# Kernel optimization log

Measured on AMD Instinct MI355X. Metric: run time of the kernel, lower is better.

## Reference

```python
import jax, jax.numpy as jnp
import numpy as np

N_SPK, N_UTT, D_EMB = 1024, 20, 512
COS_EPS = 1e-8   # torch F.cosine_similarity default eps
SIM_EPS = 1e-6   # added to cosine and inside the log, per original code


def setup_inputs() -> dict:
    key = jax.random.key(0)
    embeddings = jax.random.normal(key, (N_SPK, N_UTT, D_EMB), dtype=jnp.float32)
    w = jnp.asarray(10.0, dtype=jnp.float32)
    b = jnp.asarray(-5.0, dtype=jnp.float32)
    return {"embeddings": embeddings, "w": w, "b": b}


def reference(embeddings, w, b):
    N, M, D = embeddings.shape
    sums = embeddings.sum(axis=1)                       # [N, D]
    centroids = sums / M                                # [N, D] full centroids
    cent_excl = (sums[:, None, :] - embeddings) / (M - 1)  # [N, M, D] leave-one-out

    def _norm(x):
        return x / jnp.maximum(jnp.linalg.norm(x, axis=-1, keepdims=True), COS_EPS)

    e_n = _norm(embeddings)          # [N, M, D]
    c_n = _norm(centroids)           # [N, D]
    ce_n = _norm(cent_excl)          # [N, M, D]

    # cosine vs every speaker centroid
    cs = jnp.einsum('nmd,kd->nmk', e_n, c_n)            # [N, M, N]
    # replace same-speaker column with leave-one-out cosine
    diag = jnp.sum(e_n * ce_n, axis=-1)                 # [N, M]
    same = jnp.eye(N, dtype=bool)[:, None, :]           # [N, 1, N]
    cossim = jnp.where(same, diag[:, :, None], cs) + SIM_EPS

    sim = w * cossim + b                                # [N, M, N]
    pos = w * (diag + SIM_EPS) + b                      # sim[j, i, j]
    lse = jnp.log(jnp.sum(jnp.exp(sim), axis=-1) + SIM_EPS)  # [N, M]
    loss = jnp.sum(lse - pos)
    return loss
```

## Files before the change

kernel.cpp:

```cpp
#include <hip/hip_runtime.h>
#include <hip/hip_bf16.h>

typedef unsigned short u16;
typedef unsigned int u32;
typedef unsigned char u8;
typedef int i32x8 __attribute__((ext_vector_type(8)));
typedef float f32x4 __attribute__((ext_vector_type(4)));

#define NSPK 1024
#define NUTT 20
#define DEMB 512
#define NROW (NSPK * NUTT)

__device__ __forceinline__ uint2 pk_fp8x8(float a, float b, float c, float d,
                                          float e, float f, float g, float h) {
    int lo = __builtin_amdgcn_cvt_pk_fp8_f32(a, b, 0, 0);
    lo = __builtin_amdgcn_cvt_pk_fp8_f32(c, d, lo, 1);
    int hi = __builtin_amdgcn_cvt_pk_fp8_f32(e, f, 0, 0);
    hi = __builtin_amdgcn_cvt_pk_fp8_f32(g, h, hi, 1);
    return make_uint2((u32)lo, (u32)hi);
}

__global__ __launch_bounds__(256) void prep_f(const float* __restrict__ E,
                                              u8* __restrict__ A,
                                              u8* __restrict__ Bc,
                                              float* __restrict__ diag,
                                              float* __restrict__ csd,
                                              float* __restrict__ rs,
                                              float* __restrict__ out) {
    __shared__ float sbuf[4][DEMB];
    const int t = threadIdx.x, lane = t & 63, wv = t >> 6;
    const int n = blockIdx.x;
    const float* Eb = E + (size_t)n * (NUTT * DEMB) + (size_t)(wv * 5) * DEMB + lane * 8;

    float4 e0[5], e1[5];
    float4 p0 = {0, 0, 0, 0}, p1 = {0, 0, 0, 0};
#pragma unroll
    for (int i = 0; i < 5; ++i) {
        e0[i] = *(const float4*)(Eb + (size_t)i * DEMB);
        e1[i] = *(const float4*)(Eb + (size_t)i * DEMB + 4);
        p0.x += e0[i].x; p0.y += e0[i].y; p0.z += e0[i].z; p0.w += e0[i].w;
        p1.x += e1[i].x; p1.y += e1[i].y; p1.z += e1[i].z; p1.w += e1[i].w;
    }
    *(float4*)(&sbuf[wv][lane * 8])     = p0;
    *(float4*)(&sbuf[wv][lane * 8 + 4]) = p1;
    __syncthreads();

    float4 s0 = {0, 0, 0, 0}, s1 = {0, 0, 0, 0};
#pragma unroll
    for (int k = 0; k < 4; ++k) {
        float4 a = *(const float4*)(&sbuf[k][lane * 8]);
        float4 b = *(const float4*)(&sbuf[k][lane * 8 + 4]);
        s0.x += a.x; s0.y += a.y; s0.z += a.z; s0.w += a.w;
        s1.x += b.x; s1.y += b.y; s1.z += b.z; s1.w += b.w;
    }

    float ls = s0.x*s0.x + s0.y*s0.y + s0.z*s0.z + s0.w*s0.w
             + s1.x*s1.x + s1.y*s1.y + s1.z*s1.z + s1.w*s1.w;
#pragma unroll
    for (int o = 32; o; o >>= 1) ls += __shfl_xor(ls, o);
    const float ss = ls;
    const float rc = 1.0f / fmaxf(sqrtf(ss) * 0.05f, 1e-8f);
    const float g  = rc * 0.05f;

    ((uint2*)(Bc + (size_t)n * DEMB))[lane] =
        pk_fp8x8(s0.x * g, s0.y * g, s0.z * g, s0.w * g,
                 s1.x * g, s1.y * g, s1.z * g, s1.w * g);

#pragma unroll
    for (int i = 0; i < 5; ++i) {
        float ee = e0[i].x*e0[i].x + e0[i].y*e0[i].y + e0[i].z*e0[i].z + e0[i].w*e0[i].w
                 + e1[i].x*e1[i].x + e1[i].y*e1[i].y + e1[i].z*e1[i].z + e1[i].w*e1[i].w;
        float es = e0[i].x*s0.x + e0[i].y*s0.y + e0[i].z*s0.z + e0[i].w*s0.w
                 + e1[i].x*s1.x + e1[i].y*s1.y + e1[i].z*s1.z + e1[i].w*s1.w;
#pragma unroll
        for (int o = 32; o; o >>= 1) { ee += __shfl_xor(ee, o); es += __shfl_xor(es, o); }

        const float rne = 1.0f / fmaxf(sqrtf(ee), 1e-8f);
        const float pxx = ss - 2.f * es + ee;
        const float dg  = (es - ee) * rne / fmaxf(sqrtf(pxx), 1.9e-7f);

        const int r = n * NUTT + wv * 5 + i;
        ((uint2*)(A + (size_t)r * DEMB))[lane] =
            pk_fp8x8(e0[i].x * rne, e0[i].y * rne, e0[i].z * rne, e0[i].w * rne,
                     e1[i].x * rne, e1[i].y * rne, e1[i].z * rne, e1[i].w * rne);
        if (lane == 0) {
            diag[r] = dg;
            csd[r]  = es * g * rne;
        }
    }

    if (t < NUTT) rs[n * NUTT + t] = 0.f;
    if (n == 0 && t == 0) out[0] = 0.f;
}

__device__ __forceinline__ void async_copy16(const void* g, void* l) {
    __builtin_amdgcn_global_load_lds(
        (const __attribute__((address_space(1))) void*)g,
        (__attribute__((address_space(3))) void*)l, 16, 0, 0);
}

__global__ __launch_bounds__(256) void gemm_mx(const u8* __restrict__ A,
                                               const u8* __restrict__ Bc,
                                               const float* __restrict__ wp,
                                               const float* __restrict__ bp,
                                               float* __restrict__ rowsum) {
    __shared__ u8 As[128 * 128];
    __shared__ u8 Bs[128 * 128];
    const int t = threadIdx.x;
    const int lane = t & 63, wv = t >> 6;
    const int ml = lane & 15, q = lane >> 4;
    const int wm = wv >> 1, wn = wv & 1;
    const int tileM = blockIdx.x;
    const int tileN = blockIdx.y;

    const float w = *wp, bb = *bp;

    const u8* Ag = A + (size_t)tileM * 128 * DEMB;
    const u8* Bg = Bc + (size_t)tileN * 128 * DEMB;

    const u8* asrc[4]; const u8* bsrc[4]; u8* adst[4]; u8* bdst[4];
#pragma unroll
    for (int j = 0; j < 4; ++j) {
        const int c = t + 256 * j;
        const int r = c >> 3, kg = (c & 7) ^ (r & 7);
        asrc[j] = Ag + (size_t)r * DEMB + kg * 16;  adst[j] = As + c * 16;
        bsrc[j] = Bg + (size_t)r * DEMB + kg * 16;  bdst[j] = Bs + c * 16;
    }

    int a0[4], a1[4], b0[4], b1[4];
#pragma unroll
    for (int i = 0; i < 4; ++i) {
        const int r = wm * 64 + i * 16 + ml;
        const int c = wn * 64 + i * 16 + ml;
        a0[i] = r * 128 + (((2 * q)     ^ (r & 7)) << 4);
        a1[i] = r * 128 + (((2 * q + 1) ^ (r & 7)) << 4);
        b0[i] = c * 128 + (((2 * q)     ^ (c & 7)) << 4);
        b1[i] = c * 128 + (((2 * q + 1) ^ (c & 7)) << 4);
    }

    f32x4 acc[4][4];
#pragma unroll
    for (int i = 0; i < 4; ++i)
#pragma unroll
        for (int j = 0; j < 4; ++j) acc[i][j] = (f32x4){0.f, 0.f, 0.f, 0.f};

    for (int kt = 0; kt < DEMB; kt += 128) {
        __syncthreads();
#pragma unroll
        for (int j = 0; j < 4; ++j) async_copy16(asrc[j] + kt, adst[j]);
#pragma unroll
        for (int j = 0; j < 4; ++j) async_copy16(bsrc[j] + kt, bdst[j]);
        __syncthreads();

        i32x8 af[4], bf[4];
#pragma unroll
        for (int i = 0; i < 4; ++i) {
            uint4 x = *(const uint4*)(As + a0[i]);
            uint4 y = *(const uint4*)(As + a1[i]);
            af[i] = (i32x8){(int)x.x, (int)x.y, (int)x.z, (int)x.w,
                            (int)y.x, (int)y.y, (int)y.z, (int)y.w};
        }
#pragma unroll
        for (int j = 0; j < 4; ++j) {
            uint4 x = *(const uint4*)(Bs + b0[j]);
            uint4 y = *(const uint4*)(Bs + b1[j]);
            bf[j] = (i32x8){(int)x.x, (int)x.y, (int)x.z, (int)x.w,
                            (int)y.x, (int)y.y, (int)y.z, (int)y.w};
        }
#pragma unroll
        for (int i = 0; i < 4; ++i)
#pragma unroll
            for (int j = 0; j < 4; ++j)
                acc[i][j] = __builtin_amdgcn_mfma_scale_f32_16x16x128_f8f6f4(
                    af[i], bf[j], acc[i][j], 0, 0,
                    0, 0x7F7F7F7F, 0, 0x7F7F7F7F);
    }

#pragma unroll
    for (int i = 0; i < 4; ++i) {
        float s0 = 0.f, s1 = 0.f, s2 = 0.f, s3 = 0.f;
#pragma unroll
        for (int j = 0; j < 4; ++j) {
            s0 += __expf(fmaf(w, acc[i][j][0] + 1e-6f, bb));
            s1 += __expf(fmaf(w, acc[i][j][1] + 1e-6f, bb));
            s2 += __expf(fmaf(w, acc[i][j][2] + 1e-6f, bb));
            s3 += __expf(fmaf(w, acc[i][j][3] + 1e-6f, bb));
        }
#pragma unroll
        for (int o = 1; o < 16; o <<= 1) {
            s0 += __shfl_xor(s0, o); s1 += __shfl_xor(s1, o);
            s2 += __shfl_xor(s2, o); s3 += __shfl_xor(s3, o);
        }
        if (ml < 4) {
            float sv = (ml == 0) ? s0 : (ml == 1) ? s1 : (ml == 2) ? s2 : s3;
            int grow = tileM * 128 + wm * 64 + i * 16 + q * 4 + ml;
            atomicAdd(&rowsum[grow], sv);
        }
    }
}

__global__ __launch_bounds__(256) void finalize(const float* __restrict__ rowsum,
                                                const float* __restrict__ diag,
                                                const float* __restrict__ csd,
                                                const float* __restrict__ wp,
                                                const float* __restrict__ bp,
                                                float* __restrict__ out) {
    __shared__ float s_red[4];
    const int r = blockIdx.x * 256 + threadIdx.x;
    const float w = *wp, bb = *bp;
    const float dg = diag[r];
    const float pos = fmaf(w, dg + 1e-6f, bb);
    const float S = rowsum[r] - __expf(fmaf(w, csd[r] + 1e-6f, bb)) + __expf(pos);
    float term = __logf(S + 1e-6f) - pos;
    const int lane = threadIdx.x & 63, wv = threadIdx.x >> 6;
#pragma unroll
    for (int o = 32; o; o >>= 1) term += __shfl_xor(term, o);
    if (lane == 0) s_red[wv] = term;
    __syncthreads();
    if (threadIdx.x == 0) atomicAdd(out, s_red[0] + s_red[1] + s_red[2] + s_red[3]);
}

extern "C" void kernel_launch(void* const* d_in, const int* in_sizes, int n_in,
                              void* d_out, int out_size, void* d_ws, size_t ws_size,
                              hipStream_t stream) {
    const float* E = (const float*)d_in[0];
    const float* wp = (const float*)d_in[1];
    const float* bp = (const float*)d_in[2];
    float* out = (float*)d_out;

    char* ws = (char*)d_ws;
    u8* A      = (u8*)(ws);
    u8* Bc     = (u8*)(ws + 10485760);
    float* dg  = (float*)(ws + 11010048);
    float* cs  = (float*)(ws + 11091968);
    float* rs  = (float*)(ws + 11173888);

    prep_f<<<NSPK, 256, 0, stream>>>(E, A, Bc, dg, cs, rs, out);
    gemm_mx<<<dim3(160, 8), 256, 0, stream>>>(A, Bc, wp, bp, rs);
    finalize<<<80, 256, 0, stream>>>(rs, dg, cs, wp, bp, out);
}
```

Measured before the change: 109.1 us.

## Double-buffer GEMM LDS tiles and replace rowsum atomics with partial-sum buffer

The fp8 MFMA GEMM kernel now uses two LDS buffers per operand and issues the next K-tile's async global-to-LDS copies before computing on the current one. Explicit vmcnt waits and barriers replace the two per-iteration syncthreads, so memory loads overlap MFMA work. Row sums are no longer accumulated with atomicAdd. Each (tileN, wn) pair writes its partial sum to a 16-way buffer that finalize reduces, and this also removes the zeroing in prep. LDS use doubles to 64KB per block, which may lower occupancy, and the finalize kernel now does 16 extra reads per row.

```diff
diff --git a/kernel.cpp b/kernel.cpp
--- a/kernel.cpp
+++ b/kernel.cpp
@@ -26,7 +26,6 @@
                                               u8* __restrict__ Bc,
                                               float* __restrict__ diag,
                                               float* __restrict__ csd,
-                                              float* __restrict__ rs,
                                               float* __restrict__ out) {
     __shared__ float sbuf[4][DEMB];
     const int t = threadIdx.x, lane = t & 63, wv = t >> 6;
@@ -90,7 +89,6 @@
         }
     }
 
-    if (t < NUTT) rs[n * NUTT + t] = 0.f;
     if (n == 0 && t == 0) out[0] = 0.f;
 }
 
@@ -104,9 +102,9 @@
                                                const u8* __restrict__ Bc,
                                                const float* __restrict__ wp,
                                                const float* __restrict__ bp,
-                                               float* __restrict__ rowsum) {
-    __shared__ u8 As[128 * 128];
-    __shared__ u8 Bs[128 * 128];
+                                               float* __restrict__ rs16) {
+    __shared__ u8 As[2][128 * 128];
+    __shared__ u8 Bs[2][128 * 128];
     const int t = threadIdx.x;
     const int lane = t & 63, wv = t >> 6;
     const int ml = lane & 15, q = lane >> 4;
@@ -114,18 +112,27 @@
     const int tileM = blockIdx.x;
     const int tileN = blockIdx.y;
 
-    const float w = *wp, bb = *bp;
-
     const u8* Ag = A + (size_t)tileM * 128 * DEMB;
     const u8* Bg = Bc + (size_t)tileN * 128 * DEMB;
 
-    const u8* asrc[4]; const u8* bsrc[4]; u8* adst[4]; u8* bdst[4];
+    const u8* asrc[4]; const u8* bsrc[4]; int coff[4];
 #pragma unroll
     for (int j = 0; j < 4; ++j) {
         const int c = t + 256 * j;
         const int r = c >> 3, kg = (c & 7) ^ (r & 7);
-        asrc[j] = Ag + (size_t)r * DEMB + kg * 16;  adst[j] = As + c * 16;
-        bsrc[j] = Bg + (size_t)r * DEMB + kg * 16;  bdst[j] = Bs + c * 16;
+        asrc[j] = Ag + (size_t)r * DEMB + kg * 16;
+        bsrc[j] = Bg + (size_t)r * DEMB + kg * 16;
+        coff[j] = c * 16;
+    }
+
+#define STAGE(KT, BUF)                                                        \
+    {                                                                         \
+        _Pragma("unroll")                                                     \
+        for (int j = 0; j < 4; ++j)                                           \
+            async_copy16(asrc[j] + (KT) * 128, &As[BUF][coff[j]]);            \
+        _Pragma("unroll")                                                     \
+        for (int j = 0; j < 4; ++j)                                           \
+            async_copy16(bsrc[j] + (KT) * 128, &Bs[BUF][coff[j]]);            \
     }
 
     int a0[4], a1[4], b0[4], b1[4];
@@ -145,26 +152,19 @@
 #pragma unroll
         for (int j = 0; j < 4; ++j) acc[i][j] = (f32x4){0.f, 0.f, 0.f, 0.f};
 
-    for (int kt = 0; kt < DEMB; kt += 128) {
-        __syncthreads();
-#pragma unroll
-        for (int j = 0; j < 4; ++j) async_copy16(asrc[j] + kt, adst[j]);
-#pragma unroll
-        for (int j = 0; j < 4; ++j) async_copy16(bsrc[j] + kt, bdst[j]);
-        __syncthreads();
-
+    auto compute = [&](int buf) {
         i32x8 af[4], bf[4];
 #pragma unroll
         for (int i = 0; i < 4; ++i) {
-            uint4 x = *(const uint4*)(As + a0[i]);
-            uint4 y = *(const uint4*)(As + a1[i]);
+            uint4 x = *(const uint4*)(&As[buf][a0[i]]);
+            uint4 y = *(const uint4*)(&As[buf][a1[i]]);
             af[i] = (i32x8){(int)x.x, (int)x.y, (int)x.z, (int)x.w,
                             (int)y.x, (int)y.y, (int)y.z, (int)y.w};
         }
 #pragma unroll
         for (int j = 0; j < 4; ++j) {
-            uint4 x = *(const uint4*)(Bs + b0[j]);
-            uint4 y = *(const uint4*)(Bs + b1[j]);
+            uint4 x = *(const uint4*)(&Bs[buf][b0[j]]);
+            uint4 y = *(const uint4*)(&Bs[buf][b1[j]]);
             bf[j] = (i32x8){(int)x.x, (int)x.y, (int)x.z, (int)x.w,
                             (int)y.x, (int)y.y, (int)y.z, (int)y.w};
         }
@@ -175,8 +175,44 @@
                 acc[i][j] = __builtin_amdgcn_mfma_scale_f32_16x16x128_f8f6f4(
                     af[i], bf[j], acc[i][j], 0, 0,
                     0, 0x7F7F7F7F, 0, 0x7F7F7F7F);
-    }
-
+    };
+
+#define PHASE_END()                                            \
+    asm volatile("s_waitcnt lgkmcnt(0)" ::: "memory");         \
+    __builtin_amdgcn_sched_barrier(0);                         \
+    __builtin_amdgcn_s_barrier();                              \
+    __builtin_amdgcn_sched_barrier(0);
+
+#define WAIT_TILE(N)                                           \
+    asm volatile("s_waitcnt vmcnt(" #N ")" ::: "memory");      \
+    __builtin_amdgcn_sched_barrier(0);                         \
+    __builtin_amdgcn_s_barrier();                              \
+    __builtin_amdgcn_sched_barrier(0);
+
+    STAGE(0, 0);
+    STAGE(1, 1);
+    WAIT_TILE(8);
+    compute(0);
+    PHASE_END();
+
+    STAGE(2, 0);
+    WAIT_TILE(8);
+    compute(1);
+    PHASE_END();
+
+    STAGE(3, 1);
+    WAIT_TILE(8);
+    compute(0);
+    PHASE_END();
+
+    WAIT_TILE(0);
+    compute(1);
+
+#undef STAGE
+#undef PHASE_END
+#undef WAIT_TILE
+
+    const float w = *wp, bb = *bp;
 #pragma unroll
     for (int i = 0; i < 4; ++i) {
         float s0 = 0.f, s1 = 0.f, s2 = 0.f, s3 = 0.f;
@@ -195,12 +231,12 @@
         if (ml < 4) {
             float sv = (ml == 0) ? s0 : (ml == 1) ? s1 : (ml == 2) ? s2 : s3;
             int grow = tileM * 128 + wm * 64 + i * 16 + q * 4 + ml;
-            atomicAdd(&rowsum[grow], sv);
-        }
-    }
-}
-
-__global__ __launch_bounds__(256) void finalize(const float* __restrict__ rowsum,
+            rs16[((size_t)tileN * 2 + wn) * NROW + grow] = sv;
+        }
+    }
+}
+
+__global__ __launch_bounds__(256) void finalize(const float* __restrict__ rs16,
                                                 const float* __restrict__ diag,
                                                 const float* __restrict__ csd,
                                                 const float* __restrict__ wp,
@@ -209,9 +245,12 @@
     __shared__ float s_red[4];
     const int r = blockIdx.x * 256 + threadIdx.x;
     const float w = *wp, bb = *bp;
+    float rsum = 0.f;
+#pragma unroll
+    for (int p = 0; p < 16; ++p) rsum += rs16[(size_t)p * NROW + r];
     const float dg = diag[r];
     const float pos = fmaf(w, dg + 1e-6f, bb);
-    const float S = rowsum[r] - __expf(fmaf(w, csd[r] + 1e-6f, bb)) + __expf(pos);
+    const float S = rsum - __expf(fmaf(w, csd[r] + 1e-6f, bb)) + __expf(pos);
     float term = __logf(S + 1e-6f) - pos;
     const int lane = threadIdx.x & 63, wv = threadIdx.x >> 6;
 #pragma unroll
@@ -234,9 +273,9 @@
     u8* Bc     = (u8*)(ws + 10485760);
     float* dg  = (float*)(ws + 11010048);
     float* cs  = (float*)(ws + 11091968);
-    float* rs  = (float*)(ws + 11173888);
-
-    prep_f<<<NSPK, 256, 0, stream>>>(E, A, Bc, dg, cs, rs, out);
-    gemm_mx<<<dim3(160, 8), 256, 0, stream>>>(A, Bc, wp, bp, rs);
-    finalize<<<80, 256, 0, stream>>>(rs, dg, cs, wp, bp, out);
-}
+    float* rs16 = (float*)(ws + 11173888);
+
+    prep_f<<<NSPK, 256, 0, stream>>>(E, A, Bc, dg, cs, out);
+    gemm_mx<<<dim3(160, 8), 256, 0, stream>>>(A, Bc, wp, bp, rs16);
+    finalize<<<80, 256, 0, stream>>>(rs16, dg, cs, wp, bp, out);
+}
```

Result: no change. 107.1 us (-1.8%).

## Fuse GEMM and finalize with register-resident A rows and double-buffered B streaming

Applied to the files above, without the earlier changes.

Replaces the 2D-tiled GEMM plus separate finalize kernel with one kernel of 256 blocks. Each block keeps 80 full fp8 embedding rows resident in registers and streams all 1024 centroids through a double-buffered LDS pipeline with explicit waitcnt and barrier control. Row sums of exp stay in registers, which removes the rowsum atomics, the zeroing in prep and the finalize launch. The trade-off is one block per CU with heavy register use, and only 256 blocks to spread across the CUs.

```diff
diff --git a/kernel.cpp b/kernel.cpp
--- a/kernel.cpp
+++ b/kernel.cpp
@@ -26,7 +26,6 @@
                                               u8* __restrict__ Bc,
                                               float* __restrict__ diag,
                                               float* __restrict__ csd,
-                                              float* __restrict__ rs,
                                               float* __restrict__ out) {
     __shared__ float sbuf[4][DEMB];
     const int t = threadIdx.x, lane = t & 63, wv = t >> 6;
@@ -90,7 +89,6 @@
         }
     }
 
-    if (t < NUTT) rs[n * NUTT + t] = 0.f;
     if (n == 0 && t == 0) out[0] = 0.f;
 }
 
@@ -100,125 +98,181 @@
         (__attribute__((address_space(3))) void*)l, 16, 0, 0);
 }
 
-__global__ __launch_bounds__(256) void gemm_mx(const u8* __restrict__ A,
-                                               const u8* __restrict__ Bc,
-                                               const float* __restrict__ wp,
-                                               const float* __restrict__ bp,
-                                               float* __restrict__ rowsum) {
-    __shared__ u8 As[128 * 128];
-    __shared__ u8 Bs[128 * 128];
-    const int t = threadIdx.x;
-    const int lane = t & 63, wv = t >> 6;
+__global__ __launch_bounds__(256, 1) void gemm_fin(const u8* __restrict__ A,
+                                                   const u8* __restrict__ Bc,
+                                                   const float* __restrict__ wp,
+                                                   const float* __restrict__ bp,
+                                                   const float* __restrict__ diag,
+                                                   const float* __restrict__ csd,
+                                                   float* __restrict__ out) {
+    __shared__ u8 As[80 * DEMB];
+    __shared__ u8 Bs[2][128 * 128];
+    __shared__ float red[4][80];
+    __shared__ float s_red[4];
+    const int t = threadIdx.x, lane = t & 63, wv = t >> 6;
     const int ml = lane & 15, q = lane >> 4;
-    const int wm = wv >> 1, wn = wv & 1;
-    const int tileM = blockIdx.x;
-    const int tileN = blockIdx.y;
+    const int blk = blockIdx.x;
+    const u8* Ag = A + (size_t)blk * 80 * DEMB;
 
     const float w = *wp, bb = *bp;
-
-    const u8* Ag = A + (size_t)tileM * 128 * DEMB;
-    const u8* Bg = Bc + (size_t)tileN * 128 * DEMB;
-
-    const u8* asrc[4]; const u8* bsrc[4]; u8* adst[4]; u8* bdst[4];
+    asm volatile("s_waitcnt vmcnt(0) lgkmcnt(0)" ::: "memory");
+
+    int boff[4];
 #pragma unroll
     for (int j = 0; j < 4; ++j) {
         const int c = t + 256 * j;
         const int r = c >> 3, kg = (c & 7) ^ (r & 7);
-        asrc[j] = Ag + (size_t)r * DEMB + kg * 16;  adst[j] = As + c * 16;
-        bsrc[j] = Bg + (size_t)r * DEMB + kg * 16;  bdst[j] = Bs + c * 16;
-    }
-
-    int a0[4], a1[4], b0[4], b1[4];
-#pragma unroll
-    for (int i = 0; i < 4; ++i) {
-        const int r = wm * 64 + i * 16 + ml;
-        const int c = wn * 64 + i * 16 + ml;
-        a0[i] = r * 128 + (((2 * q)     ^ (r & 7)) << 4);
-        a1[i] = r * 128 + (((2 * q + 1) ^ (r & 7)) << 4);
-        b0[i] = c * 128 + (((2 * q)     ^ (c & 7)) << 4);
-        b1[i] = c * 128 + (((2 * q + 1) ^ (c & 7)) << 4);
-    }
-
-    f32x4 acc[4][4];
-#pragma unroll
-    for (int i = 0; i < 4; ++i)
-#pragma unroll
-        for (int j = 0; j < 4; ++j) acc[i][j] = (f32x4){0.f, 0.f, 0.f, 0.f};
-
-    for (int kt = 0; kt < DEMB; kt += 128) {
-        __syncthreads();
-#pragma unroll
-        for (int j = 0; j < 4; ++j) async_copy16(asrc[j] + kt, adst[j]);
-#pragma unroll
-        for (int j = 0; j < 4; ++j) async_copy16(bsrc[j] + kt, bdst[j]);
-        __syncthreads();
-
-        i32x8 af[4], bf[4];
-#pragma unroll
-        for (int i = 0; i < 4; ++i) {
-            uint4 x = *(const uint4*)(As + a0[i]);
-            uint4 y = *(const uint4*)(As + a1[i]);
-            af[i] = (i32x8){(int)x.x, (int)x.y, (int)x.z, (int)x.w,
-                            (int)y.x, (int)y.y, (int)y.z, (int)y.w};
-        }
-#pragma unroll
-        for (int j = 0; j < 4; ++j) {
-            uint4 x = *(const uint4*)(Bs + b0[j]);
-            uint4 y = *(const uint4*)(Bs + b1[j]);
-            bf[j] = (i32x8){(int)x.x, (int)x.y, (int)x.z, (int)x.w,
-                            (int)y.x, (int)y.y, (int)y.z, (int)y.w};
-        }
-#pragma unroll
-        for (int i = 0; i < 4; ++i)
-#pragma unroll
-            for (int j = 0; j < 4; ++j)
-                acc[i][j] = __builtin_amdgcn_mfma_scale_f32_16x16x128_f8f6f4(
-                    af[i], bf[j], acc[i][j], 0, 0,
-                    0, 0x7F7F7F7F, 0, 0x7F7F7F7F);
-    }
-
-#pragma unroll
-    for (int i = 0; i < 4; ++i) {
-        float s0 = 0.f, s1 = 0.f, s2 = 0.f, s3 = 0.f;
-#pragma unroll
-        for (int j = 0; j < 4; ++j) {
-            s0 += __expf(fmaf(w, acc[i][j][0] + 1e-6f, bb));
-            s1 += __expf(fmaf(w, acc[i][j][1] + 1e-6f, bb));
-            s2 += __expf(fmaf(w, acc[i][j][2] + 1e-6f, bb));
-            s3 += __expf(fmaf(w, acc[i][j][3] + 1e-6f, bb));
-        }
+        boff[j] = r * DEMB + kg * 16;
+    }
+
+    auto stageB = [&](int tileN, int kt, u8* buf) {
+#pragma unroll
+        for (int j = 0; j < 4; ++j)
+            async_copy16(Bc + (size_t)tileN * (128 * DEMB) + kt * 128 + boff[j],
+                         buf + t * 16 + j * 4096);
+    };
+
+#pragma unroll
+    for (int jj = 0; jj < 10; ++jj) {
+        const int c = t + 256 * jj;
+        const int r = c >> 5, sl = c & 31;
+        async_copy16(Ag + (size_t)r * DEMB + ((sl ^ (r & 31)) << 4),
+                     As + t * 16 + jj * 4096);
+    }
+    stageB(0, 0, Bs[0]);
+    stageB(0, 1, Bs[1]);
+    asm volatile("s_waitcnt vmcnt(4)" ::: "memory");
+    __builtin_amdgcn_sched_barrier(0);
+    __builtin_amdgcn_s_barrier();
+    __builtin_amdgcn_sched_barrier(0);
+
+    i32x8 a[5][4];
+#pragma unroll
+    for (int m = 0; m < 5; ++m) {
+        const int r = m * 16 + ml;
+#pragma unroll
+        for (int kt = 0; kt < 4; ++kt) {
+            const int sl0 = (kt * 8 + 2 * q)     ^ (r & 31);
+            const int sl1 = (kt * 8 + 2 * q + 1) ^ (r & 31);
+            uint4 x = *(const uint4*)(As + r * DEMB + (sl0 << 4));
+            uint4 y = *(const uint4*)(As + r * DEMB + (sl1 << 4));
+            a[m][kt] = (i32x8){(int)x.x, (int)x.y, (int)x.z, (int)x.w,
+                               (int)y.x, (int)y.y, (int)y.z, (int)y.w};
+        }
+    }
+    asm volatile("s_waitcnt lgkmcnt(0)" ::: "memory");
+    __builtin_amdgcn_sched_barrier(0);
+
+    f32x4 acc[5][2], rowpart[5];
+#pragma unroll
+    for (int m = 0; m < 5; ++m) {
+        acc[m][0] = (f32x4){0.f, 0.f, 0.f, 0.f};
+        acc[m][1] = (f32x4){0.f, 0.f, 0.f, 0.f};
+        rowpart[m] = (f32x4){0.f, 0.f, 0.f, 0.f};
+    }
+
+    int bo0[2], bo1[2];
+#pragma unroll
+    for (int nf = 0; nf < 2; ++nf) {
+        const int c = wv * 32 + nf * 16 + ml;
+        bo0[nf] = c * 128 + (((2 * q)     ^ (c & 7)) << 4);
+        bo1[nf] = c * 128 + (((2 * q + 1) ^ (c & 7)) << 4);
+    }
+
+    for (int tileN = 0; tileN < 8; ++tileN) {
+#pragma unroll
+        for (int kt = 0; kt < 4; ++kt) {
+            const u8* bufc = Bs[kt & 1];
+            i32x8 bf[2];
+#pragma unroll
+            for (int nf = 0; nf < 2; ++nf) {
+                uint4 x = *(const uint4*)(bufc + bo0[nf]);
+                uint4 y = *(const uint4*)(bufc + bo1[nf]);
+                bf[nf] = (i32x8){(int)x.x, (int)x.y, (int)x.z, (int)x.w,
+                                 (int)y.x, (int)y.y, (int)y.z, (int)y.w};
+            }
+            asm volatile("s_waitcnt lgkmcnt(0)" ::: "memory");
+            __builtin_amdgcn_sched_barrier(0);
+#pragma unroll
+            for (int m = 0; m < 5; ++m)
+#pragma unroll
+                for (int nf = 0; nf < 2; ++nf)
+                    acc[m][nf] = __builtin_amdgcn_mfma_scale_f32_16x16x128_f8f6f4(
+                        a[m][kt], bf[nf], acc[m][nf], 0, 0,
+                        0, 0x7F7F7F7F, 0, 0x7F7F7F7F);
+
+            __builtin_amdgcn_sched_barrier(0);
+            __builtin_amdgcn_s_barrier();
+            __builtin_amdgcn_sched_barrier(0);
+
+            if (kt < 2 || tileN < 7)
+                stageB(tileN + (kt >= 2), (kt + 2) & 3, (u8*)Bs[kt & 1]);
+
+            if (kt == 3) {
+#pragma unroll
+                for (int m = 0; m < 5; ++m) {
+#pragma unroll
+                    for (int r = 0; r < 4; ++r)
+                        rowpart[m][r] += __expf(fmaf(w, acc[m][0][r] + 1e-6f, bb))
+                                       + __expf(fmaf(w, acc[m][1][r] + 1e-6f, bb));
+                    acc[m][0] = (f32x4){0.f, 0.f, 0.f, 0.f};
+                    acc[m][1] = (f32x4){0.f, 0.f, 0.f, 0.f};
+                }
+            }
+
+            if (kt == 2) {
+                if (tileN == 7) { asm volatile("s_waitcnt vmcnt(0)" ::: "memory"); }
+                else           { asm volatile("s_waitcnt vmcnt(4)" ::: "memory"); }
+                __builtin_amdgcn_sched_barrier(0);
+                __builtin_amdgcn_s_barrier();
+                __builtin_amdgcn_sched_barrier(0);
+            } else if (kt == 3) {
+                if (tileN < 7) {
+                    asm volatile("s_waitcnt vmcnt(4)" ::: "memory");
+                    __builtin_amdgcn_sched_barrier(0);
+                    __builtin_amdgcn_s_barrier();
+                    __builtin_amdgcn_sched_barrier(0);
+                }
+            } else {
+                asm volatile("s_waitcnt vmcnt(4)" ::: "memory");
+                __builtin_amdgcn_sched_barrier(0);
+                __builtin_amdgcn_s_barrier();
+                __builtin_amdgcn_sched_barrier(0);
+            }
+        }
+    }
+
+#pragma unroll
+    for (int m = 0; m < 5; ++m)
 #pragma unroll
         for (int o = 1; o < 16; o <<= 1) {
-            s0 += __shfl_xor(s0, o); s1 += __shfl_xor(s1, o);
-            s2 += __shfl_xor(s2, o); s3 += __shfl_xor(s3, o);
-        }
-        if (ml < 4) {
-            float sv = (ml == 0) ? s0 : (ml == 1) ? s1 : (ml == 2) ? s2 : s3;
-            int grow = tileM * 128 + wm * 64 + i * 16 + q * 4 + ml;
-            atomicAdd(&rowsum[grow], sv);
-        }
-    }
-}
-
-__global__ __launch_bounds__(256) void finalize(const float* __restrict__ rowsum,
-                                                const float* __restrict__ diag,
-                                                const float* __restrict__ csd,
-                                                const float* __restrict__ wp,
-                                                const float* __restrict__ bp,
-                                                float* __restrict__ out) {
-    __shared__ float s_red[4];
-    const int r = blockIdx.x * 256 + threadIdx.x;
-    const float w = *wp, bb = *bp;
-    const float dg = diag[r];
-    const float pos = fmaf(w, dg + 1e-6f, bb);
-    const float S = rowsum[r] - __expf(fmaf(w, csd[r] + 1e-6f, bb)) + __expf(pos);
-    float term = __logf(S + 1e-6f) - pos;
-    const int lane = threadIdx.x & 63, wv = threadIdx.x >> 6;
+            rowpart[m][0] += __shfl_xor(rowpart[m][0], o);
+            rowpart[m][1] += __shfl_xor(rowpart[m][1], o);
+            rowpart[m][2] += __shfl_xor(rowpart[m][2], o);
+            rowpart[m][3] += __shfl_xor(rowpart[m][3], o);
+        }
+    if (ml == 0) {
+#pragma unroll
+        for (int m = 0; m < 5; ++m)
+#pragma unroll
+            for (int r = 0; r < 4; ++r)
+                red[wv][m * 16 + q * 4 + r] = rowpart[m][r];
+    }
+    __syncthreads();
+
+    float term = 0.f;
+    if (t < 80) {
+        const float rsum = red[0][t] + red[1][t] + red[2][t] + red[3][t];
+        const int row = blk * 80 + t;
+        const float pos = fmaf(w, diag[row] + 1e-6f, bb);
+        const float S = rsum - __expf(fmaf(w, csd[row] + 1e-6f, bb)) + __expf(pos);
+        term = __logf(S + 1e-6f) - pos;
+    }
 #pragma unroll
     for (int o = 32; o; o >>= 1) term += __shfl_xor(term, o);
     if (lane == 0) s_red[wv] = term;
     __syncthreads();
-    if (threadIdx.x == 0) atomicAdd(out, s_red[0] + s_red[1] + s_red[2] + s_red[3]);
+    if (t == 0) atomicAdd(out, s_red[0] + s_red[1] + s_red[2] + s_red[3]);
 }
 
 extern "C" void kernel_launch(void* const* d_in, const int* in_sizes, int n_in,
@@ -234,9 +288,7 @@
     u8* Bc     = (u8*)(ws + 10485760);
     float* dg  = (float*)(ws + 11010048);
     float* cs  = (float*)(ws + 11091968);
-    float* rs  = (float*)(ws + 11173888);
-
-    prep_f<<<NSPK, 256, 0, stream>>>(E, A, Bc, dg, cs, rs, out);
-    gemm_mx<<<dim3(160, 8), 256, 0, stream>>>(A, Bc, wp, bp, rs);
-    finalize<<<80, 256, 0, stream>>>(rs, dg, cs, wp, bp, out);
-}
+
+    prep_f<<<NSPK, 256, 0, stream>>>(E, A, Bc, dg, cs, out);
+    gemm_fin<<<256, 256, 0, stream>>>(A, Bc, wp, bp, dg, cs, out);
+}
```

After: 107.9 us. Within noise of the previous version (-1.1%).
